# Performance work log

Measured on AMD Instinct MI355X. Metric: run time of the kernel, lower is better.

## Reference

```python
import jax, jax.numpy as jnp
import numpy as np


def setup_inputs() -> dict:
    key = jax.random.key(0)
    k1, k2, k3, k4 = jax.random.split(key, 4)
    B, S, D_in, D_state, D_out = 8, 2048, 1024, 1024, 1024
    x = jax.random.normal(k1, (B, S, D_in), dtype=jnp.float32)
    # A ~ rand * 0.1 (as in torch init)
    A = jax.random.uniform(k2, (D_state,), dtype=jnp.float32) * 0.1
    # B.weight ~ U(-0.01, 0.01)
    B_w = jax.random.uniform(k3, (D_state, D_in), dtype=jnp.float32, minval=-0.01, maxval=0.01)
    # linear_out: default torch Linear init (kaiming-uniform-ish); just use small uniform
    bound = 1.0 / np.sqrt(D_state)
    kw, kb = jax.random.split(k4)
    Wo = jax.random.uniform(kw, (D_out, D_state), dtype=jnp.float32, minval=-bound, maxval=bound)
    bo = jax.random.uniform(kb, (D_out,), dtype=jnp.float32, minval=-bound, maxval=bound)
    return {"x": x, "A": A, "B_w": B_w, "Wo": Wo, "bo": bo}


def reference(x, A, B_w, Wo, bo):
    # x: (B, S, D_in)
    Bsz = x.shape[0]
    D_state = A.shape[0]
    exp_decay = jnp.exp(-jnp.minimum(A, 10.0))  # (D_state,)
    # Precompute input projection in one batched matmul: (B, S, D_state)
    Bx = jnp.einsum("bsi,ni->bsn", x, B_w)

    def step(state, bx_t):
        # state: (B, D_state); bx_t: (B, D_state)
        state = jnp.tanh(exp_decay * state + bx_t)
        return state, state

    init = jnp.zeros((Bsz, D_state), dtype=x.dtype)
    # scan over time axis: move S to leading axis
    _, h = jax.lax.scan(step, init, jnp.swapaxes(Bx, 0, 1))  # h: (S, B, D_state)
    h = jnp.swapaxes(h, 0, 1)  # (B, S, D_state)
    out = jnp.einsum("bsn,on->bso", h, Wo) + bo
    return out
```

## Files before the change

### kernel.cpp

```cpp
#include <hip/hip_runtime.h>
#include <stdint.h>


typedef __attribute__((ext_vector_type(8))) short bf16x8;
typedef __attribute__((ext_vector_type(4))) float f32x4;
typedef __attribute__((ext_vector_type(8))) unsigned short u16x8;

#define C2F 2.88539008177792681472f
#define LOG2E 1.44269504088896340736f

static __device__ __forceinline__ unsigned short f2b(float f) {
  unsigned u = __builtin_bit_cast(unsigned, f);
  unsigned r = 0x7FFFu + ((u >> 16) & 1u);
  return (unsigned short)((u + r) >> 16);
}

static __device__ __forceinline__ void gload_lds16(const void* g, void* l) {
  __builtin_amdgcn_global_load_lds(
      (const __attribute__((address_space(1))) void*)(uintptr_t)g,
      (__attribute__((address_space(3))) void*)(unsigned)(uintptr_t)l,
      16, 0, 0);
}

__global__ __launch_bounds__(256) void cvt_f32_bf16(const float* __restrict__ in,
                                                    unsigned short* __restrict__ out,
                                                    float scale, int n8) {
  int i = blockIdx.x * 256 + threadIdx.x;
  if (i >= n8) return;
  const float4* p = (const float4*)in;
  float4 v0 = p[2 * (size_t)i];
  float4 v1 = p[2 * (size_t)i + 1];
  u16x8 o;
  o[0] = f2b(v0.x * scale); o[1] = f2b(v0.y * scale);
  o[2] = f2b(v0.z * scale); o[3] = f2b(v0.w * scale);
  o[4] = f2b(v1.x * scale); o[5] = f2b(v1.y * scale);
  o[6] = f2b(v1.z * scale); o[7] = f2b(v1.w * scale);
  *(u16x8*)(out + 8 * (size_t)i) = o;
}

__global__ __launch_bounds__(256) void dkc_kernel(const float* __restrict__ Av,
                                                  float* __restrict__ dkc, int n) {
  int i = blockIdx.x * 256 + threadIdx.x;
  if (i >= n) return;
  float a = fminf(Av[i], 10.0f);
  dkc[i] = C2F * __builtin_amdgcn_exp2f(-a * LOG2E);
}

__global__ __launch_bounds__(256) void bias2_kernel(const float* __restrict__ Wo,
                                                    const float* __restrict__ bo,
                                                    float* __restrict__ bias2) {
  const int o = blockIdx.x * 4 + (threadIdx.x >> 6);
  const int lane = threadIdx.x & 63;
  const float4* row = (const float4*)(Wo + (size_t)o * 1024);
  float s = 0.0f;
#pragma unroll
  for (int k = 0; k < 4; ++k) {
    float4 v = row[lane + k * 64];
    s += v.x + v.y + v.z + v.w;
  }
#pragma unroll
  for (int off = 32; off; off >>= 1) s += __shfl_down(s, off);
  if (lane == 0) bias2[o] = s + bo[o];
}

template <int MODE>
__global__ __launch_bounds__(512, 2) void gemm256(const unsigned short* __restrict__ A,
                                                  const unsigned short* __restrict__ B,
                                                  float* __restrict__ C,
                                                  const float* __restrict__ bv,
                                                  int M, int N, int K) {
  __shared__ char lds[4][2][16384];
  const int tid = threadIdx.x;
  const int wave = tid >> 6, lane = tid & 63;
  const int wr = wave >> 2, wc = wave & 3;

  const int nbn = N >> 8;
  const int per = gridDim.x >> 3;
  const int tilei = (blockIdx.x & 7) * per + (blockIdx.x >> 3);
  const int m0 = (tilei / nbn) << 8;
  const int n0 = (tilei % nbn) << 8;

  int soff[2];
#pragma unroll
  for (int i = 0; i < 2; ++i) {
    int o = i * 8192 + wave * 1024 + lane * 16;
    int rp = o >> 7;
    int p = ((o >> 4) & 7) ^ (rp & 7);
    int row = rp * 2 + (p >> 2);
    int chunk = p & 3;
    soff[i] = row * K + chunk * 8;
  }
  const unsigned short* Abase = A + (size_t)m0 * K;
  const unsigned short* Bbase = B + (size_t)n0 * K;

#define STAGEP(SLOT, K0S)                                                         \
  {                                                                               \
    _Pragma("unroll") for (int i = 0; i < 2; ++i) {                               \
      gload_lds16(Abase + (K0S) + soff[i], &lds[SLOT][0][i * 8192 + wave * 1024]); \
      gload_lds16(Bbase + (K0S) + soff[i], &lds[SLOT][1][i * 8192 + wave * 1024]); \
    }                                                                             \
  }

  const int l15 = lane & 15, ck = lane >> 4;
  const int ra = wr * 128 + l15;
  const int rb = wc * 64 + l15;
  const int baseA = (ra >> 1) * 128 + ((((ra & 1) << 2) + ck) ^ ((ra >> 1) & 7)) * 16;
  const int baseB = (rb >> 1) * 128 + ((((rb & 1) << 2) + ck) ^ ((rb >> 1) & 7)) * 16;

  f32x4 accT[4][8] = {};
  bf16x8 rA[8], rB[4];

#define MFMA_(a_, b_, c_) __builtin_amdgcn_mfma_f32_16x16x32_bf16(a_, b_, c_, 0, 0, 0)

#define PHASE(SLOT, WAITN, DOSTAGE, K0S)                                          \
  {                                                                               \
    asm volatile("s_waitcnt vmcnt(" WAITN ")" ::: "memory");                      \
    __builtin_amdgcn_s_barrier();                                                 \
    _Pragma("unroll") for (int f = 0; f < 4; ++f)                                 \
        rB[f] = *(const bf16x8*)(&lds[SLOT][1][baseB + f * 1024]);                \
    _Pragma("unroll") for (int f = 0; f < 8; ++f)                                 \
        rA[f] = *(const bf16x8*)(&lds[SLOT][0][baseA + f * 1024]);                \
    asm volatile("s_waitcnt lgkmcnt(0)" ::: "memory");                            \
    __builtin_amdgcn_sched_barrier(0);                                            \
    __builtin_amdgcn_s_setprio(1);                                                \
    _Pragma("unroll") for (int mf = 0; mf < 8; ++mf)                              \
      _Pragma("unroll") for (int nf = 0; nf < 4; ++nf)                            \
        accT[nf][mf] = MFMA_(rB[nf], rA[mf], accT[nf][mf]);                       \
    __builtin_amdgcn_s_setprio(0);                                                \
    __builtin_amdgcn_s_barrier();                                                 \
    if (DOSTAGE) STAGEP(SLOT, K0S);                                               \
  }

  const int T = K / 64;

  STAGEP(0, 0); STAGEP(1, 32); STAGEP(2, 64); STAGEP(3, 96);

  for (int t = 0; t < T - 2; ++t) {
    const int sa = (t & 1) * 2;
    PHASE(sa,     "12", true, t * 64 + 128);
    PHASE(sa + 1, "12", true, t * 64 + 160);
  }
  {
    const int sa = ((T - 2) & 1) * 2;
    PHASE(sa,     "12", false, 0);
    PHASE(sa + 1, "8",  false, 0);
  }
  {
    const int sa = ((T - 1) & 1) * 2;
    PHASE(sa,     "4",  false, 0);
    PHASE(sa + 1, "0",  false, 0);
  }

#undef PHASE
#undef STAGEP
#undef MFMA_

  const int cm = lane & 15;
  const int cn = (lane >> 4) * 4;
#pragma unroll
  for (int nf = 0; nf < 4; ++nf) {
    const int gn = n0 + wc * 64 + nf * 16 + cn;
    const f32x4 bb = *(const f32x4*)(bv + gn);
#pragma unroll
    for (int mf = 0; mf < 8; ++mf) {
      const int gm = m0 + wr * 128 + mf * 16 + cm;
      f32x4 v = accT[nf][mf];
      if (MODE == 0) v = v * C2F + bb; else v = v + bb;
      *(f32x4*)(C + (size_t)gm * N + gn) = v;
    }
  }
}

__global__ __launch_bounds__(256) void scan_kernel(const float* __restrict__ Bx,
                                                   const float* __restrict__ Av,
                                                   unsigned short* __restrict__ h) {
  constexpr int S = 2048, D = 1024, CHUNK = 256, W = 384;
  const int bid = blockIdx.x;
  const int half = bid & 1;
  const int chunk = (bid >> 1) & 7;
  const int b = bid >> 4;
  const int p = half * 256 + threadIdx.x;
  const unsigned n0 = 2u * p;

  const float2 av = *(const float2*)(Av + n0);
  const float m2dk0 = -2.0f * C2F * __builtin_amdgcn_exp2f(-fminf(av.x, 10.0f) * LOG2E);
  const float m2dk1 = -2.0f * C2F * __builtin_amdgcn_exp2f(-fminf(av.y, 10.0f) * LOG2E);

  const unsigned base = (unsigned)b * (S * D) + n0;
  const int t_store0 = chunk * CHUNK;
  const int t_start = (chunk * CHUNK - W) < 0 ? 0 : (chunk * CHUNK - W);
  const int t_end = t_store0 + CHUNK;

  float2 A[8], Bf[8];
#pragma unroll
  for (int j = 0; j < 8; ++j) A[j] = *(const float2*)(Bx + base + (unsigned)(t_start + j) * D);
#pragma unroll
  for (int j = 0; j < 8; ++j) Bf[j] = *(const float2*)(Bx + base + (unsigned)(t_start + 8 + j) * D);

  float r0 = 0.5f, r1 = 0.5f;

#define STEP2(CV)                                         \
  {                                                       \
    float w0 = fmaf(m2dk0, r0, (CV).x);                   \
    float w1 = fmaf(m2dk1, r1, (CV).y);                   \
    float e0 = __builtin_amdgcn_exp2f(w0);                \
    float e1 = __builtin_amdgcn_exp2f(w1);                \
    r0 = __builtin_amdgcn_rcpf(e0 + 1.0f);                \
    r1 = __builtin_amdgcn_rcpf(e1 + 1.0f);                \
  }

#define STORE2(T_)                                                        \
  {                                                                       \
    unsigned pk;                                                          \
    asm("v_cvt_pk_bf16_f32 %0, %1, %2" : "=v"(pk) : "v"(r0), "v"(r1));    \
    *(unsigned*)(h + base + (unsigned)(T_) * D) = pk;                     \
  }

  for (int t0 = t_start; t0 < t_store0; t0 += 16) {
#pragma unroll
    for (int j = 0; j < 8; ++j) STEP2(A[j]);
#pragma unroll
    for (int j = 0; j < 8; ++j) A[j] = *(const float2*)(Bx + base + (unsigned)(t0 + 16 + j) * D);
#pragma unroll
    for (int j = 0; j < 8; ++j) STEP2(Bf[j]);
#pragma unroll
    for (int j = 0; j < 8; ++j) Bf[j] = *(const float2*)(Bx + base + (unsigned)(t0 + 24 + j) * D);
  }
  for (int t0 = t_store0; t0 < t_end; t0 += 16) {
#pragma unroll
    for (int j = 0; j < 8; ++j) { STEP2(A[j]); STORE2(t0 + j); }
    if (t0 + 16 < t_end) {
#pragma unroll
      for (int j = 0; j < 8; ++j) A[j] = *(const float2*)(Bx + base + (unsigned)(t0 + 16 + j) * D);
    }
#pragma unroll
    for (int j = 0; j < 8; ++j) { STEP2(Bf[j]); STORE2(t0 + 8 + j); }
    if (t0 + 24 < t_end) {
#pragma unroll
      for (int j = 0; j < 8; ++j) Bf[j] = *(const float2*)(Bx + base + (unsigned)(t0 + 24 + j) * D);
    }
  }
#undef STEP2
#undef STORE2
}

extern "C" void kernel_launch(void* const* d_in, const int* in_sizes, int n_in,
                              void* d_out, int out_size, void* d_ws, size_t ws_size,
                              hipStream_t stream) {
  const float* x  = (const float*)d_in[0];
  const float* Av = (const float*)d_in[1];
  const float* Bw = (const float*)d_in[2];
  const float* Wo = (const float*)d_in[3];
  const float* bo = (const float*)d_in[4];
  float* out = (float*)d_out;

  const int Bsz = 8, S = 2048, Din = 1024, Dst = 1024, Dout = 1024;
  const int M = Bsz * S;

  char* ws = (char*)d_ws;
  unsigned short* x_bf  = (unsigned short*)ws;
  unsigned short* r_bf  = (unsigned short*)(ws + (size_t)M * Din * 2);
  unsigned short* Bw_bf = (unsigned short*)(ws + (size_t)M * Din * 4);
  unsigned short* Wo_bf = (unsigned short*)(ws + (size_t)M * Din * 4 + (size_t)Dst * Din * 2);
  float* dkc   = (float*)(ws + (size_t)M * Din * 4 + (size_t)Dst * Din * 4);
  float* bias2 = dkc + Dst;

  float* Bx = out;

  { int n8 = M * Din / 8;
    cvt_f32_bf16<<<(n8 + 255) / 256, 256, 0, stream>>>(x, x_bf, 1.0f, n8); }
  { int n8 = Dst * Din / 8;
    cvt_f32_bf16<<<(n8 + 255) / 256, 256, 0, stream>>>(Bw, Bw_bf, 1.0f, n8); }
  { int n8 = Dout * Dst / 8;
    cvt_f32_bf16<<<(n8 + 255) / 256, 256, 0, stream>>>(Wo, Wo_bf, -2.0f, n8); }
  dkc_kernel<<<4, 256, 0, stream>>>(Av, dkc, Dst);
  bias2_kernel<<<Dout / 4, 256, 0, stream>>>(Wo, bo, bias2);

  gemm256<0><<<dim3((M / 256) * (Dst / 256)), 512, 0, stream>>>(x_bf, Bw_bf, Bx, dkc, M, Dst, Din);
  scan_kernel<<<dim3(128), 256, 0, stream>>>(Bx, Av, r_bf);
  gemm256<1><<<dim3((M / 256) * (Dout / 256)), 512, 0, stream>>>(r_bf, Wo_bf, out, bias2, M, Dout, Dst);
}
```

Before: 147.5 us.

## Store Bx intermediate as bf16 and fold decay scaling into scan

```diff
diff --git a/kernel.cpp b/kernel.cpp
--- a/kernel.cpp
+++ b/kernel.cpp
@@ -38,14 +38,6 @@
   *(u16x8*)(out + 8 * (size_t)i) = o;
 }
 
-__global__ __launch_bounds__(256) void dkc_kernel(const float* __restrict__ Av,
-                                                  float* __restrict__ dkc, int n) {
-  int i = blockIdx.x * 256 + threadIdx.x;
-  if (i >= n) return;
-  float a = fminf(Av[i], 10.0f);
-  dkc[i] = C2F * __builtin_amdgcn_exp2f(-a * LOG2E);
-}
-
 __global__ __launch_bounds__(256) void bias2_kernel(const float* __restrict__ Wo,
                                                     const float* __restrict__ bo,
                                                     float* __restrict__ bias2) {
@@ -66,7 +58,7 @@
 template <int MODE>
 __global__ __launch_bounds__(512, 2) void gemm256(const unsigned short* __restrict__ A,
                                                   const unsigned short* __restrict__ B,
-                                                  float* __restrict__ C,
+                                                  void* __restrict__ Cv,
                                                   const float* __restrict__ bv,
                                                   int M, int N, int K) {
   __shared__ char lds[4][2][16384];
@@ -160,18 +152,26 @@
 #pragma unroll
   for (int nf = 0; nf < 4; ++nf) {
     const int gn = n0 + wc * 64 + nf * 16 + cn;
-    const f32x4 bb = *(const f32x4*)(bv + gn);
 #pragma unroll
     for (int mf = 0; mf < 8; ++mf) {
       const int gm = m0 + wr * 128 + mf * 16 + cm;
       f32x4 v = accT[nf][mf];
-      if (MODE == 0) v = v * C2F + bb; else v = v + bb;
-      *(f32x4*)(C + (size_t)gm * N + gn) = v;
+      if constexpr (MODE == 0) {
+        unsigned lo, hi;
+        asm("v_cvt_pk_bf16_f32 %0, %1, %2" : "=v"(lo) : "v"(v[0]), "v"(v[1]));
+        asm("v_cvt_pk_bf16_f32 %0, %1, %2" : "=v"(hi) : "v"(v[2]), "v"(v[3]));
+        uint2 st; st.x = lo; st.y = hi;
+        *(uint2*)((unsigned short*)Cv + (size_t)gm * N + gn) = st;
+      } else {
+        const f32x4 bb = *(const f32x4*)(bv + gn);
+        v = v + bb;
+        *(f32x4*)((float*)Cv + (size_t)gm * N + gn) = v;
+      }
     }
   }
 }
 
-__global__ __launch_bounds__(256) void scan_kernel(const float* __restrict__ Bx,
+__global__ __launch_bounds__(256) void scan_kernel(const unsigned* __restrict__ Bxp,
                                                    const float* __restrict__ Av,
                                                    unsigned short* __restrict__ h) {
   constexpr int S = 2048, D = 1024, CHUNK = 256, W = 384;
@@ -185,19 +185,31 @@
   const float2 av = *(const float2*)(Av + n0);
   const float m2dk0 = -2.0f * C2F * __builtin_amdgcn_exp2f(-fminf(av.x, 10.0f) * LOG2E);
   const float m2dk1 = -2.0f * C2F * __builtin_amdgcn_exp2f(-fminf(av.y, 10.0f) * LOG2E);
-
-  const unsigned base = (unsigned)b * (S * D) + n0;
+  const float dkc0 = -0.5f * m2dk0;
+  const float dkc1 = -0.5f * m2dk1;
+
+  const unsigned base = (unsigned)b * (S * D / 2) + p;
+  const unsigned hbase = (unsigned)b * (S * D) + n0;
   const int t_store0 = chunk * CHUNK;
   const int t_start = (chunk * CHUNK - W) < 0 ? 0 : (chunk * CHUNK - W);
   const int t_end = t_store0 + CHUNK;
-
-  float2 A[8], Bf[8];
-#pragma unroll
-  for (int j = 0; j < 8; ++j) A[j] = *(const float2*)(Bx + base + (unsigned)(t_start + j) * D);
-#pragma unroll
-  for (int j = 0; j < 8; ++j) Bf[j] = *(const float2*)(Bx + base + (unsigned)(t_start + 8 + j) * D);
+  constexpr unsigned DW = D / 2;
+
+  unsigned uA[8], uB[8];
+#pragma unroll
+  for (int j = 0; j < 8; ++j) uA[j] = Bxp[base + (unsigned)(t_start + j) * DW];
+#pragma unroll
+  for (int j = 0; j < 8; ++j) uB[j] = Bxp[base + (unsigned)(t_start + 8 + j) * DW];
 
   float r0 = 0.5f, r1 = 0.5f;
+
+#define PREP(CV, U)                                                       \
+  {                                                                       \
+    float lo = __builtin_bit_cast(float, (U) << 16);                      \
+    float hi = __builtin_bit_cast(float, (U) & 0xFFFF0000u);              \
+    (CV).x = fmaf(C2F, lo, dkc0);                                         \
+    (CV).y = fmaf(C2F, hi, dkc1);                                         \
+  }
 
 #define STEP2(CV)                                         \
   {                                                       \
@@ -213,33 +225,44 @@
   {                                                                       \
     unsigned pk;                                                          \
     asm("v_cvt_pk_bf16_f32 %0, %1, %2" : "=v"(pk) : "v"(r0), "v"(r1));    \
-    *(unsigned*)(h + base + (unsigned)(T_) * D) = pk;                     \
+    *(unsigned*)(h + hbase + (unsigned)(T_) * D) = pk;                    \
   }
 
   for (int t0 = t_start; t0 < t_store0; t0 += 16) {
-#pragma unroll
-    for (int j = 0; j < 8; ++j) STEP2(A[j]);
-#pragma unroll
-    for (int j = 0; j < 8; ++j) A[j] = *(const float2*)(Bx + base + (unsigned)(t0 + 16 + j) * D);
-#pragma unroll
-    for (int j = 0; j < 8; ++j) STEP2(Bf[j]);
-#pragma unroll
-    for (int j = 0; j < 8; ++j) Bf[j] = *(const float2*)(Bx + base + (unsigned)(t0 + 24 + j) * D);
+    float2 c[8];
+#pragma unroll
+    for (int j = 0; j < 8; ++j) PREP(c[j], uA[j]);
+#pragma unroll
+    for (int j = 0; j < 8; ++j) uA[j] = Bxp[base + (unsigned)(t0 + 16 + j) * DW];
+#pragma unroll
+    for (int j = 0; j < 8; ++j) STEP2(c[j]);
+#pragma unroll
+    for (int j = 0; j < 8; ++j) PREP(c[j], uB[j]);
+#pragma unroll
+    for (int j = 0; j < 8; ++j) uB[j] = Bxp[base + (unsigned)(t0 + 24 + j) * DW];
+#pragma unroll
+    for (int j = 0; j < 8; ++j) STEP2(c[j]);
   }
   for (int t0 = t_store0; t0 < t_end; t0 += 16) {
-#pragma unroll
-    for (int j = 0; j < 8; ++j) { STEP2(A[j]); STORE2(t0 + j); }
+    float2 c[8];
+#pragma unroll
+    for (int j = 0; j < 8; ++j) PREP(c[j], uA[j]);
     if (t0 + 16 < t_end) {
 #pragma unroll
-      for (int j = 0; j < 8; ++j) A[j] = *(const float2*)(Bx + base + (unsigned)(t0 + 16 + j) * D);
+      for (int j = 0; j < 8; ++j) uA[j] = Bxp[base + (unsigned)(t0 + 16 + j) * DW];
     }
 #pragma unroll
-    for (int j = 0; j < 8; ++j) { STEP2(Bf[j]); STORE2(t0 + 8 + j); }
+    for (int j = 0; j < 8; ++j) { STEP2(c[j]); STORE2(t0 + j); }
+#pragma unroll
+    for (int j = 0; j < 8; ++j) PREP(c[j], uB[j]);
     if (t0 + 24 < t_end) {
 #pragma unroll
-      for (int j = 0; j < 8; ++j) Bf[j] = *(const float2*)(Bx + base + (unsigned)(t0 + 24 + j) * D);
+      for (int j = 0; j < 8; ++j) uB[j] = Bxp[base + (unsigned)(t0 + 24 + j) * DW];
     }
-  }
+#pragma unroll
+    for (int j = 0; j < 8; ++j) { STEP2(c[j]); STORE2(t0 + 8 + j); }
+  }
+#undef PREP
 #undef STEP2
 #undef STORE2
 }
@@ -262,10 +285,9 @@
   unsigned short* r_bf  = (unsigned short*)(ws + (size_t)M * Din * 2);
   unsigned short* Bw_bf = (unsigned short*)(ws + (size_t)M * Din * 4);
   unsigned short* Wo_bf = (unsigned short*)(ws + (size_t)M * Din * 4 + (size_t)Dst * Din * 2);
-  float* dkc   = (float*)(ws + (size_t)M * Din * 4 + (size_t)Dst * Din * 4);
-  float* bias2 = dkc + Dst;
-
-  float* Bx = out;
+  float* bias2 = (float*)(ws + (size_t)M * Din * 4 + (size_t)Dst * Din * 4);
+
+  unsigned short* Bx_bf = (unsigned short*)d_out;
 
   { int n8 = M * Din / 8;
     cvt_f32_bf16<<<(n8 + 255) / 256, 256, 0, stream>>>(x, x_bf, 1.0f, n8); }
@@ -273,10 +295,11 @@
     cvt_f32_bf16<<<(n8 + 255) / 256, 256, 0, stream>>>(Bw, Bw_bf, 1.0f, n8); }
   { int n8 = Dout * Dst / 8;
     cvt_f32_bf16<<<(n8 + 255) / 256, 256, 0, stream>>>(Wo, Wo_bf, -2.0f, n8); }
-  dkc_kernel<<<4, 256, 0, stream>>>(Av, dkc, Dst);
   bias2_kernel<<<Dout / 4, 256, 0, stream>>>(Wo, bo, bias2);
 
-  gemm256<0><<<dim3((M / 256) * (Dst / 256)), 512, 0, stream>>>(x_bf, Bw_bf, Bx, dkc, M, Dst, Din);
-  scan_kernel<<<dim3(128), 256, 0, stream>>>(Bx, Av, r_bf);
-  gemm256<1><<<dim3((M / 256) * (Dout / 256)), 512, 0, stream>>>(r_bf, Wo_bf, out, bias2, M, Dout, Dst);
-}
+  gemm256<0><<<dim3((M / 256) * (Dst / 256)), 512, 0, stream>>>(x_bf, Bw_bf, (void*)Bx_bf,
+                                                                nullptr, M, Dst, Din);
+  scan_kernel<<<dim3(128), 256, 0, stream>>>((const unsigned*)Bx_bf, Av, r_bf);
+  gemm256<1><<<dim3((M / 256) * (Dout / 256)), 512, 0, stream>>>(r_bf, Wo_bf, (void*)out,
+                                                                 bias2, M, Dout, Dst);
+}
```

Result: faster. 136.2 us (-7.6%).
